# Kernel tuning notes

Measured on AMD Instinct MI355X. Metric: run time of the kernel, lower is better.

The kernel has to match this reference:

```python
import jax, jax.numpy as jnp
import numpy as np

LOSS_CUTOFF = 100000.0
EPS = 1e-08

B, S, A = 512, 512, 200


def setup_inputs() -> dict:
    key = jax.random.key(0)
    k1, k2, k3, k4 = jax.random.split(key, 4)
    logits = jax.random.normal(k1, (B, S, A), dtype=jnp.float32)
    actions = jax.random.randint(k2, (B, S), 0, A, dtype=jnp.int64)
    rewards = jax.random.uniform(k3, (B, S), dtype=jnp.float32)
    terminals = jax.random.uniform(k4, (B, S), dtype=jnp.float32)
    return {"logits": logits, "actions": actions, "rewards": rewards, "terminals": terminals}


def reference(logits, actions, rewards, terminals):
    # log_p: [B, S, A], masked by (1 - terminals)
    log_p = jax.nn.log_softmax(logits, axis=2) * (1.0 - terminals)[:, :, None]
    # gather per-timestep action log-prob: [B, S] -> total_logp: [B]
    action_logp = jnp.take_along_axis(log_p, actions[:, :, None], axis=2)[..., 0]
    total_logp = -jnp.sum(action_logp, axis=1)  # [B]
    total_rewards = jnp.sum(rewards, axis=1)    # [B]
    # 'mean' branch: masked mean over total_logp < loss_cutoff
    prod = total_logp * total_rewards
    mask = total_logp < LOSS_CUTOFF
    cnt = jnp.sum(mask.astype(prod.dtype))
    rewardloss_mean = jnp.sum(jnp.where(mask, prod, 0.0)) / cnt
    mean_loss = rewardloss_mean / (jnp.mean(jnp.abs(total_rewards)) + EPS)
    return mean_loss
```

## Files before the change

kernel.cpp:

```cpp
#include <hip/hip_runtime.h>
#include <hip/hip_bf16.h>
#include <math.h>


#define BDIM 512
#define SDIM 512
#define ADIM 200
#define ROWS_PER_WAVE 8
#define WAVES_PER_BLOCK 4
#define ROWS_PER_BLOCK (ROWS_PER_WAVE * WAVES_PER_BLOCK)
#define NBLOCKS ((BDIM * SDIM) / ROWS_PER_BLOCK)

typedef float nf4 __attribute__((ext_vector_type(4)));

__device__ __forceinline__ float dpp_reduce_add(float x) {
    int t;
    t = __builtin_amdgcn_update_dpp(0, __float_as_int(x), 0x111, 0xf, 0xf, true); x += __int_as_float(t);
    t = __builtin_amdgcn_update_dpp(0, __float_as_int(x), 0x112, 0xf, 0xf, true); x += __int_as_float(t);
    t = __builtin_amdgcn_update_dpp(0, __float_as_int(x), 0x114, 0xf, 0xf, true); x += __int_as_float(t);
    t = __builtin_amdgcn_update_dpp(0, __float_as_int(x), 0x118, 0xf, 0xf, true); x += __int_as_float(t);
    t = __builtin_amdgcn_update_dpp(0, __float_as_int(x), 0x142, 0xa, 0xf, true); x += __int_as_float(t);
    t = __builtin_amdgcn_update_dpp(0, __float_as_int(x), 0x143, 0xc, 0xf, true); x += __int_as_float(t);
    return x;
}

__global__ __launch_bounds__(256, 4) void pg_row_kernel(
    const float* __restrict__ logits,
    const int*   __restrict__ actions,
    const float* __restrict__ rewards,
    const float* __restrict__ terminals,
    float* __restrict__ ws_logp,
    float* __restrict__ ws_rew)
{
    const int lane = threadIdx.x & 63;
    const int wave = threadIdx.x >> 6;
    const int row0 = blockIdx.x * ROWS_PER_BLOCK + wave * ROWS_PER_WAVE;
    const int b    = blockIdx.x >> 4;

    const int cl = (lane < 50) ? lane : 49;

    const int4*   ap = (const int4*)  (actions   + row0);
    const float4* tp = (const float4*)(terminals + row0);
    const float4* rp = (const float4*)(rewards   + row0);
    const int4   a03 = ap[0], a47 = ap[1];
    const float4 t03 = tp[0], t47 = tp[1];
    const float4 r03 = rp[0], r47 = rp[1];
    const int   a[ROWS_PER_WAVE]  = {a03.x, a03.y, a03.z, a03.w, a47.x, a47.y, a47.z, a47.w};
    const float tm[ROWS_PER_WAVE] = {t03.x, t03.y, t03.z, t03.w, t47.x, t47.y, t47.z, t47.w};
    const float rw[ROWS_PER_WAVE] = {r03.x, r03.y, r03.z, r03.w, r47.x, r47.y, r47.z, r47.w};

    nf4 v[ROWS_PER_WAVE];
    #pragma unroll
    for (int i = 0; i < ROWS_PER_WAVE; ++i) {
        const nf4* rowp = (const nf4*)(logits + (size_t)(row0 + i) * ADIM);
        v[i] = __builtin_nontemporal_load(rowp + cl);
    }

    float acc_logp = 0.0f, acc_rew = 0.0f;
    #pragma unroll
    for (int i = 0; i < ROWS_PER_WAVE; ++i) {
        const int   sub  = a[i] & 3;
        const float cand = (sub == 0) ? v[i].x : (sub == 1) ? v[i].y
                         : (sub == 2) ? v[i].z : v[i].w;
        const float xa   = __shfl(cand, a[i] >> 2);

        float s = __expf(v[i].x) + __expf(v[i].y) +
                  __expf(v[i].z) + __expf(v[i].w);
        s = (lane < 50) ? s : 0.0f;
        const float tot  = dpp_reduce_add(s);
        const float etot = __int_as_float(
            __builtin_amdgcn_readlane(__float_as_int(tot), 63));

        acc_logp += (xa - __logf(etot)) * (1.0f - tm[i]);
        acc_rew  += rw[i];
    }

    __shared__ float s_logp[WAVES_PER_BLOCK], s_rew[WAVES_PER_BLOCK];
    if (lane == 0) { s_logp[wave] = acc_logp; s_rew[wave] = acc_rew; }
    __syncthreads();
    if (threadIdx.x == 0) {
        float tl = 0.0f, tr = 0.0f;
        #pragma unroll
        for (int w = 0; w < WAVES_PER_BLOCK; ++w) { tl += s_logp[w]; tr += s_rew[w]; }
        atomicAdd(&ws_logp[b], tl);
        atomicAdd(&ws_rew[b],  tr);
    }
}

__global__ __launch_bounds__(512) void pg_final_kernel(
    const float* __restrict__ ws_logp,
    const float* __restrict__ ws_rew,
    float* __restrict__ out)
{
    const int tid  = threadIdx.x;
    const int lane = tid & 63;
    const int wave = tid >> 6;

    const float total_logp = -ws_logp[tid];
    const float total_rew  =  ws_rew[tid];

    float mp   = (total_logp < 100000.0f) ? total_logp * total_rew : 0.0f;
    float cnt  = (total_logp < 100000.0f) ? 1.0f : 0.0f;
    float arew = fabsf(total_rew);

    #pragma unroll
    for (int off = 32; off >= 1; off >>= 1) {
        mp   += __shfl_down(mp,   off);
        cnt  += __shfl_down(cnt,  off);
        arew += __shfl_down(arew, off);
    }

    __shared__ float s_mp[8], s_cnt[8], s_ab[8];
    if (lane == 0) { s_mp[wave] = mp; s_cnt[wave] = cnt; s_ab[wave] = arew; }
    __syncthreads();
    if (tid == 0) {
        float smp = 0.0f, scnt = 0.0f, sab = 0.0f;
        #pragma unroll
        for (int i = 0; i < 8; ++i) { smp += s_mp[i]; scnt += s_cnt[i]; sab += s_ab[i]; }
        const float rewardloss_mean = smp / scnt;
        out[0] = rewardloss_mean / (sab / (float)BDIM + 1e-8f);
    }
}

extern "C" void kernel_launch(void* const* d_in, const int* in_sizes, int n_in,
                              void* d_out, int out_size, void* d_ws, size_t ws_size,
                              hipStream_t stream) {
    const float* logits    = (const float*)d_in[0];
    const int*   actions   = (const int*)  d_in[1];
    const float* rewards   = (const float*)d_in[2];
    const float* terminals = (const float*)d_in[3];

    float* ws_logp = (float*)d_ws;
    float* ws_rew  = ws_logp + BDIM;

    (void)hipMemsetAsync(d_ws, 0, 2 * BDIM * sizeof(float), stream);

    pg_row_kernel<<<NBLOCKS, 256, 0, stream>>>(
        logits, actions, rewards, terminals, ws_logp, ws_rew);

    pg_final_kernel<<<1, 512, 0, stream>>>(ws_logp, ws_rew, (float*)d_out);
}
```

Before: 277.2 us.

## Replace per-batch atomics with per-block slots and scalarize per-row loads

```diff
diff --git a/kernel.cpp b/kernel.cpp
--- a/kernel.cpp
+++ b/kernel.cpp
@@ -10,6 +10,7 @@
 #define WAVES_PER_BLOCK 4
 #define ROWS_PER_BLOCK (ROWS_PER_WAVE * WAVES_PER_BLOCK)
 #define NBLOCKS ((BDIM * SDIM) / ROWS_PER_BLOCK)
+#define BLOCKS_PER_B (SDIM / ROWS_PER_BLOCK)
 
 typedef float nf4 __attribute__((ext_vector_type(4)));
 
@@ -24,30 +25,28 @@
     return x;
 }
 
-__global__ __launch_bounds__(256, 4) void pg_row_kernel(
+__global__ __launch_bounds__(256, 8) void pg_row_kernel(
     const float* __restrict__ logits,
     const int*   __restrict__ actions,
     const float* __restrict__ rewards,
     const float* __restrict__ terminals,
-    float* __restrict__ ws_logp,
-    float* __restrict__ ws_rew)
+    float* __restrict__ slots)
 {
     const int lane = threadIdx.x & 63;
     const int wave = threadIdx.x >> 6;
-    const int row0 = blockIdx.x * ROWS_PER_BLOCK + wave * ROWS_PER_WAVE;
-    const int b    = blockIdx.x >> 4;
+    const int row0 = __builtin_amdgcn_readfirstlane(
+        blockIdx.x * ROWS_PER_BLOCK + wave * ROWS_PER_WAVE);
 
     const int cl = (lane < 50) ? lane : 49;
 
-    const int4*   ap = (const int4*)  (actions   + row0);
-    const float4* tp = (const float4*)(terminals + row0);
-    const float4* rp = (const float4*)(rewards   + row0);
-    const int4   a03 = ap[0], a47 = ap[1];
-    const float4 t03 = tp[0], t47 = tp[1];
-    const float4 r03 = rp[0], r47 = rp[1];
-    const int   a[ROWS_PER_WAVE]  = {a03.x, a03.y, a03.z, a03.w, a47.x, a47.y, a47.z, a47.w};
-    const float tm[ROWS_PER_WAVE] = {t03.x, t03.y, t03.z, t03.w, t47.x, t47.y, t47.z, t47.w};
-    const float rw[ROWS_PER_WAVE] = {r03.x, r03.y, r03.z, r03.w, r47.x, r47.y, r47.z, r47.w};
+    int   a [ROWS_PER_WAVE];
+    float tm[ROWS_PER_WAVE], rw[ROWS_PER_WAVE];
+    #pragma unroll
+    for (int i = 0; i < ROWS_PER_WAVE; ++i) {
+        a [i] = actions  [row0 + i];
+        tm[i] = terminals[row0 + i];
+        rw[i] = rewards  [row0 + i];
+    }
 
     nf4 v[ROWS_PER_WAVE];
     #pragma unroll
@@ -62,7 +61,8 @@
         const int   sub  = a[i] & 3;
         const float cand = (sub == 0) ? v[i].x : (sub == 1) ? v[i].y
                          : (sub == 2) ? v[i].z : v[i].w;
-        const float xa   = __shfl(cand, a[i] >> 2);
+        const float xa   = __int_as_float(
+            __builtin_amdgcn_readlane(__float_as_int(cand), a[i] >> 2));
 
         float s = __expf(v[i].x) + __expf(v[i].y) +
                   __expf(v[i].z) + __expf(v[i].w);
@@ -82,22 +82,27 @@
         float tl = 0.0f, tr = 0.0f;
         #pragma unroll
         for (int w = 0; w < WAVES_PER_BLOCK; ++w) { tl += s_logp[w]; tr += s_rew[w]; }
-        atomicAdd(&ws_logp[b], tl);
-        atomicAdd(&ws_rew[b],  tr);
+        slots[blockIdx.x]           = tl;
+        slots[NBLOCKS + blockIdx.x] = tr;
     }
 }
 
 __global__ __launch_bounds__(512) void pg_final_kernel(
-    const float* __restrict__ ws_logp,
-    const float* __restrict__ ws_rew,
+    const float* __restrict__ slots,
     float* __restrict__ out)
 {
-    const int tid  = threadIdx.x;
-    const int lane = tid & 63;
-    const int wave = tid >> 6;
+    const int b    = threadIdx.x;
+    const int lane = b & 63;
+    const int wave = b >> 6;
 
-    const float total_logp = -ws_logp[tid];
-    const float total_rew  =  ws_rew[tid];
+    float tl = 0.0f, tr = 0.0f;
+    #pragma unroll
+    for (int j = 0; j < BLOCKS_PER_B; ++j) {
+        tl += slots[b * BLOCKS_PER_B + j];
+        tr += slots[NBLOCKS + b * BLOCKS_PER_B + j];
+    }
+    const float total_logp = -tl;
+    const float total_rew  =  tr;
 
     float mp   = (total_logp < 100000.0f) ? total_logp * total_rew : 0.0f;
     float cnt  = (total_logp < 100000.0f) ? 1.0f : 0.0f;
@@ -113,7 +118,7 @@
     __shared__ float s_mp[8], s_cnt[8], s_ab[8];
     if (lane == 0) { s_mp[wave] = mp; s_cnt[wave] = cnt; s_ab[wave] = arew; }
     __syncthreads();
-    if (tid == 0) {
+    if (threadIdx.x == 0) {
         float smp = 0.0f, scnt = 0.0f, sab = 0.0f;
         #pragma unroll
         for (int i = 0; i < 8; ++i) { smp += s_mp[i]; scnt += s_cnt[i]; sab += s_ab[i]; }
@@ -130,13 +135,10 @@
     const float* rewards   = (const float*)d_in[2];
     const float* terminals = (const float*)d_in[3];
 
-    float* ws_logp = (float*)d_ws;
-    float* ws_rew  = ws_logp + BDIM;
-
-    (void)hipMemsetAsync(d_ws, 0, 2 * BDIM * sizeof(float), stream);
+    float* slots = (float*)d_ws;
 
     pg_row_kernel<<<NBLOCKS, 256, 0, stream>>>(
-        logits, actions, rewards, terminals, ws_logp, ws_rew);
+        logits, actions, rewards, terminals, slots);
 
-    pg_final_kernel<<<1, 512, 0, stream>>>(ws_logp, ws_rew, (float*)d_out);
+    pg_final_kernel<<<1, 512, 0, stream>>>(slots, (float*)d_out);
 }
```

After: 273.0 us. No clear change (-1.5%).
